# Performance work log

Hardware: AMD Instinct MI355X
Metric: run time of the kernel (lower is better)

Reference implementation:

```python
import jax, jax.numpy as jnp
import numpy as np

B, T, D, H = 1, 2049, 1024, 16
HD = D // H                      # head_dim = 64
MAX_SEQ = 1025
L = 2 * MAX_SEQ - 1              # = T (required by the module's relative shift)

def setup_inputs() -> dict:
    key = jax.random.key(0)
    ks = jax.random.split(key, 12)
    s = 0.02
    return {
        'q': jax.random.normal(ks[0], (B, T, D), dtype=jnp.float32),
        'k': jax.random.normal(ks[1], (B, T, D), dtype=jnp.float32),
        'v': jax.random.normal(ks[2], (B, T, D), dtype=jnp.float32),
        'mask': jnp.tril(jnp.ones((1, 1, T, T), dtype=jnp.int32)),  # causal
        'Wq_w': jax.random.normal(ks[3], (D, D), dtype=jnp.float32) * s,
        'Wq_b': jnp.zeros((D,), dtype=jnp.float32),
        'Wk_w': jax.random.normal(ks[4], (D, D), dtype=jnp.float32) * s,
        'Wk_b': jnp.zeros((D,), dtype=jnp.float32),
        'Wv_w': jax.random.normal(ks[5], (D, D), dtype=jnp.float32) * s,
        'Wv_b': jnp.zeros((D,), dtype=jnp.float32),
        'Er': jax.random.normal(ks[6], (L, HD), dtype=jnp.float32),
        'Wo_w': jax.random.normal(ks[7], (D, D), dtype=jnp.float32) * s,
        'Wo_b': jnp.zeros((D,), dtype=jnp.float32),
    }

def reference(q, k, v, mask, Wq_w, Wq_b, Wk_w, Wk_b, Wv_w, Wv_b, Er, Wo_w, Wo_b):
    b, t, d = q.shape
    def proj(x, w, bias):
        # nn.Linear: x @ W^T + b ; then (B,T,H,HD) -> (B,H,T,HD)
        return (x @ w.T + bias).reshape(b, t, H, HD).transpose(0, 2, 1, 3)
    qh = proj(q, Wq_w, Wq_b)
    kh = proj(k, Wk_w, Wk_b)
    vh = proj(v, Wv_w, Wv_b)
    scores = jnp.einsum('bhtd,bhsd->bhts', qh, kh)          # (B,H,T,T)
    QEr = jnp.einsum('bhtd,ld->bhtl', qh, Er)               # (B,H,T,L) with L == T
    # _relative_shift: pad a zero row on seq dim then drop first row ->
    # row i becomes QEr row i+1, last row zeros (faithful to torch code)
    rel = jnp.concatenate([QEr[:, :, 1:, :], jnp.zeros_like(QEr[:, :, :1, :])], axis=2)
    scores = scores + rel
    scores = jnp.where(mask[:, :, :t, :t] == 0, -jnp.inf, scores)
    attn = jax.nn.softmax(scores / (HD ** 0.5), axis=-1)
    ctx = jnp.einsum('bhts,bhsd->bthd', attn, vh).reshape(b, t, d)
    return ctx @ Wo_w.T + Wo_b
```

## Files before the change

kernel.cpp:

```cpp
#include <hip/hip_runtime.h>
#include <hip/hip_bf16.h>
#include <math.h>

constexpr int T_SEQ = 2049;
constexpr int D_MODEL = 1024;
constexpr int N_HEAD = 16;
constexpr int HEAD_DIM = 64;
constexpr int VT_STRIDE = 2112;
constexpr int T1_ROWS = 1152;

typedef __attribute__((ext_vector_type(8))) short short8;
typedef __attribute__((ext_vector_type(4))) short short4v;
typedef __attribute__((ext_vector_type(4))) float floatx4;

__device__ inline void load_lds16(const void* g, void* l) {
  __builtin_amdgcn_global_load_lds(
      (const __attribute__((address_space(1))) unsigned int*)g,
      (__attribute__((address_space(3))) unsigned int*)l, 16, 0, 0);
}

__device__ inline short8 cvt8_bf16(const float* p) {
  float4 a = *(const float4*)p, b = *(const float4*)(p + 4);
  __hip_bfloat16 t[8] = {__float2bfloat16(a.x), __float2bfloat16(a.y),
                         __float2bfloat16(a.z), __float2bfloat16(a.w),
                         __float2bfloat16(b.x), __float2bfloat16(b.y),
                         __float2bfloat16(b.z), __float2bfloat16(b.w)};
  return *(const short8*)t;
}

__device__ inline float bf2f(__hip_bfloat16 x) { return __bfloat162float(x); }

__global__ __launch_bounds__(256) void cast_all(
    const float* __restrict__ q, const float* __restrict__ k,
    const float* __restrict__ v, const float* __restrict__ wq,
    const float* __restrict__ wk, const float* __restrict__ wv,
    const float* __restrict__ wo, const float* __restrict__ er,
    __hip_bfloat16* __restrict__ qo, __hip_bfloat16* __restrict__ ko,
    __hip_bfloat16* __restrict__ vo, __hip_bfloat16* __restrict__ wqo,
    __hip_bfloat16* __restrict__ wko, __hip_bfloat16* __restrict__ wvo,
    __hip_bfloat16* __restrict__ woo, __hip_bfloat16* __restrict__ ero) {
  const int z = blockIdx.y;
  const float* in;
  __hip_bfloat16* out;
  int n;
  switch (z) {
    case 0: in = q; out = qo; n = T_SEQ * D_MODEL; break;
    case 1: in = k; out = ko; n = T_SEQ * D_MODEL; break;
    case 2: in = v; out = vo; n = T_SEQ * D_MODEL; break;
    case 3: in = wq; out = wqo; n = D_MODEL * D_MODEL; break;
    case 4: in = wk; out = wko; n = D_MODEL * D_MODEL; break;
    case 5: in = wv; out = wvo; n = D_MODEL * D_MODEL; break;
    case 6: in = wo; out = woo; n = D_MODEL * D_MODEL; break;
    default: in = er; out = ero; n = T_SEQ * HEAD_DIM; break;
  }
  const int i = (blockIdx.x * 256 + threadIdx.x) * 8;
  if (i + 8 > n) return;
  *(short8*)(out + i) = cvt8_bf16(in + i);
}

template <int BM, int BN, int OUTK>
__global__ __launch_bounds__(256) void mfma_gemm(
    const __hip_bfloat16* __restrict__ A0, const __hip_bfloat16* __restrict__ A1,
    const __hip_bfloat16* __restrict__ A2, const __hip_bfloat16* __restrict__ W0,
    const __hip_bfloat16* __restrict__ W1, const __hip_bfloat16* __restrict__ W2,
    const float* __restrict__ bias0, const float* __restrict__ bias1,
    const float* __restrict__ bias2, void* C0, void* C1, void* C2, int M) {
  constexpr int K = D_MODEL;
  constexpr int MT = BM / 32;
  constexpr int NT = BN / 32;
  __shared__ __align__(16) __hip_bfloat16 As[2][BM * 64];
  __shared__ __align__(16) __hip_bfloat16 Bs[2][BN * 64];

  const int z = blockIdx.z;
  const short* A = (const short*)(z == 0 ? A0 : z == 1 ? A1 : A2);
  const short* W = (const short*)(z == 0 ? W0 : z == 1 ? W1 : W2);
  const float* bias = z == 0 ? bias0 : z == 1 ? bias1 : bias2;
  void* C = z == 0 ? C0 : z == 1 ? C1 : C2;

  const int tid = threadIdx.x;
  const int wave = tid >> 6, lane = tid & 63;
  const int col = lane & 15, quad = lane >> 4;
  const int wm = wave >> 1, wn = wave & 1;
  const int m0 = blockIdx.y * BM, n0 = blockIdx.x * BN;

  const int srow = lane >> 3;
  const int sslot = lane & 7;
  const int sch = sslot ^ srow;

  floatx4 acc[MT][NT];
#pragma unroll
  for (int i = 0; i < MT; i++)
#pragma unroll
    for (int j = 0; j < NT; j++) acc[i][j] = (floatx4){0.f, 0.f, 0.f, 0.f};

#define GSTAGE(K0, BUF)                                                     \
  {                                                                         \
    _Pragma("unroll") for (int ii = 0; ii < BM / 32; ii++) {                \
      const int rb = (wave * (BM / 32) + ii) * 8;                           \
      const int am = min(m0 + rb + srow, M - 1);                            \
      load_lds16(A + (size_t)am * K + (K0) + sch * 8,                       \
                 (char*)&As[BUF][0] + rb * 128);                            \
    }                                                                       \
    _Pragma("unroll") for (int ii = 0; ii < BN / 32; ii++) {                \
      const int rb = (wave * (BN / 32) + ii) * 8;                           \
      const int bn = n0 + rb + srow;                                        \
      load_lds16(W + (size_t)bn * K + (K0) + sch * 8,                       \
                 (char*)&Bs[BUF][0] + rb * 128);                            \
    }                                                                       \
  }

  GSTAGE(0, 0)
  int buf = 0;

  for (int kb = 0; kb < K / 64; ++kb, buf ^= 1) {
    __syncthreads();
    if (kb + 1 < K / 64) GSTAGE((kb + 1) * 64, buf ^ 1)

    const __hip_bfloat16* as = &As[buf][0];
    const __hip_bfloat16* bs = &Bs[buf][0];
#pragma unroll
    for (int kk = 0; kk < 2; kk++) {
      short8 af[MT], bf[NT];
#pragma unroll
      for (int t = 0; t < MT; t++) {
        const int ra = wm * (BM / 2) + t * 16 + col;
        af[t] = *(const short8*)(as + ra * 64 + ((kk * 4 + quad) ^ (ra & 7)) * 8);
      }
#pragma unroll
      for (int t = 0; t < NT; t++) {
        const int rb = wn * (BN / 2) + t * 16 + col;
        bf[t] = *(const short8*)(bs + rb * 64 + ((kk * 4 + quad) ^ (rb & 7)) * 8);
      }
#pragma unroll
      for (int mt = 0; mt < MT; mt++)
#pragma unroll
        for (int nt = 0; nt < NT; nt++)
          acc[mt][nt] = __builtin_amdgcn_mfma_f32_16x16x32_bf16(af[mt], bf[nt],
                                                                acc[mt][nt], 0, 0, 0);
    }
  }

#pragma unroll
  for (int mt = 0; mt < MT; mt++) {
    const int mb = m0 + wm * (BM / 2) + mt * 16 + quad * 4;
#pragma unroll
    for (int nt = 0; nt < NT; nt++) {
      const int n = n0 + wn * (BN / 2) + nt * 16 + col;
      if (OUTK == 2 && z == 2) {
        __hip_bfloat16 pb[4];
#pragma unroll
        for (int r = 0; r < 4; r++)
          pb[r] = __float2bfloat16(acc[mt][nt][r] + bias[n]);
        __hip_bfloat16* vrow = (__hip_bfloat16*)C + (size_t)n * VT_STRIDE;
        if (mb + 4 <= M) {
          *(short4v*)(vrow + mb) = *(const short4v*)pb;
        } else {
#pragma unroll
          for (int r = 0; r < 4; r++)
            if (mb + r < M) vrow[mb + r] = pb[r];
        }
      } else {
#pragma unroll
        for (int r = 0; r < 4; r++) {
          const int m = mb + r;
          if (m >= M) continue;
          const float val = acc[mt][nt][r] + bias[n];
          if (OUTK == 0) {
            ((float*)C)[(size_t)m * D_MODEL + n] = val;
          } else {
            const int h = n >> 6, hd = n & 63;
            ((__hip_bfloat16*)C)[((size_t)h * T_SEQ + m) * HEAD_DIM + hd] =
                __float2bfloat16(val);
          }
        }
      }
    }
  }
}

__global__ __launch_bounds__(512, 4) void flash_attn(
    const __hip_bfloat16* __restrict__ qh, const __hip_bfloat16* __restrict__ kh,
    const __hip_bfloat16* __restrict__ er, const __hip_bfloat16* __restrict__ vt,
    __hip_bfloat16* __restrict__ ctx, __hip_bfloat16* __restrict__ O0,
    __hip_bfloat16* __restrict__ O1, float* __restrict__ l0g,
    float* __restrict__ l1g) {
  __shared__ __align__(16) __hip_bfloat16 Ks[2][64 * 128];
  __shared__ __align__(16) __hip_bfloat16 Vs[2][64 * 64];
  __shared__ __align__(16) __hip_bfloat16 Ps[8][1024];

  const int tid = threadIdx.x;
  const int h = blockIdx.y;
  const int b = blockIdx.x;

  const int qt = (b < 8) ? b : 8 + ((b - 8) >> 1);
  const int tq0 = qt * 128;
  const int jmax = min(tq0 + 127, T_SEQ - 1) >> 6;
  int j0, j1;
  bool alt;
  if (b < 8) {
    j0 = 0; j1 = jmax; alt = false;
  } else {
    const int mid = (jmax + 1) >> 1;
    alt = (b - 8) & 1;
    j0 = alt ? mid : 0;
    j1 = alt ? jmax : mid - 1;
  }

  const int wave = tid >> 6;
  const int lane = tid & 63;
  const int col = lane & 15;
  const int quad = lane >> 4;

  const short* qplane = (const short*)(qh + (size_t)h * T_SEQ * HEAD_DIM);
  const short* kplane = (const short*)(kh + (size_t)h * T_SEQ * HEAD_DIM);
  const short* eplane = (const short*)er;
  const short* vplane = (const short*)(vt + (size_t)h * HEAD_DIM * VT_STRIDE);

  const int t_abs = tq0 + wave * 16 + col;
  const int tload = min(t_abs, T_SEQ - 1);
  const bool hiz = (t_abs >= T_SEQ - 1);
  short8 aq[4];
#pragma unroll
  for (int kc = 0; kc < 4; kc++) {
    short8 v = *(const short8*)(qplane + (size_t)tload * 64 + kc * 32 + quad * 8);
    if (kc >= 2 && hiz) v = (short8){0, 0, 0, 0, 0, 0, 0, 0};
    aq[kc] = v;
  }

  floatx4 o[4];
  float l_lane = 0.f;
#pragma unroll
  for (int i = 0; i < 4; i++) o[i] = (floatx4){0.f, 0.f, 0.f, 0.f};

  const int tstrip = tq0 + wave * 16;
  __hip_bfloat16* psw = &Ps[wave][0];

#define STAGE_TILE(JJ, BUF)                                                        \
  {                                                                                \
    const int s0_ = (JJ) * 64;                                                     \
    _Pragma("unroll") for (int ii = 0; ii < 2; ii++) {                             \
      const int i_ = wave * 2 + ii;                                                \
      const int r_ = i_ * 4 + (lane >> 4);                                         \
      const int sl_ = lane & 15;                                                   \
      const int g_ = (sl_ & 8) | ((sl_ ^ (r_ & 7)) & 7);                           \
      const int s_ = min(s0_ + r_, T_SEQ - 1);                                     \
      const short* src_ = (g_ < 8) ? (kplane + (size_t)s_ * 64 + g_ * 8)           \
                                   : (eplane + (size_t)s_ * 64 + (g_ - 8) * 8);    \
      load_lds16(src_, (char*)&Ks[BUF][0] + i_ * 1024);                            \
    }                                                                              \
    {                                                                              \
      const int d_ = wave * 8 + (lane >> 3);                                       \
      const int sl_ = lane & 7;                                                    \
      const int g_ = sl_ ^ (d_ & 7);                                               \
      load_lds16(vplane + (size_t)d_ * VT_STRIDE + s0_ + g_ * 8,                   \
                 (char*)&Vs[BUF][0] + wave * 1024);                                \
    }                                                                              \
  }

  STAGE_TILE(j0, 0)
  int buf = 0;

  for (int j = j0; j <= j1; ++j, buf ^= 1) {
    __syncthreads();
    if (j < j1) STAGE_TILE(j + 1, buf ^ 1)

    const int s0 = j * 64;
    if (s0 > tstrip + 15) continue;

    const __hip_bfloat16* ks = &Ks[buf][0];
    const __hip_bfloat16* vs = &Vs[buf][0];

    floatx4 sacc[4];
#pragma unroll
    for (int st = 0; st < 4; st++) {
      floatx4 c = {0.f, 0.f, 0.f, 0.f};
      const int row = st * 16 + col;
#pragma unroll
      for (int kc = 0; kc < 4; kc++) {
        const int ch = kc * 4 + quad;
        const int slot = (ch & 8) | ((ch ^ (row & 7)) & 7);
        short8 ka = *(const short8*)(ks + row * 128 + slot * 8);
        c = __builtin_amdgcn_mfma_f32_16x16x32_bf16(ka, aq[kc], c, 0, 0, 0);
      }
      sacc[st] = c;
    }

    if (s0 + 63 > tstrip) {
#pragma unroll
      for (int st = 0; st < 4; st++) {
        const int sbase = s0 + st * 16 + quad * 4;
#pragma unroll
        for (int r = 0; r < 4; r++)
          if (sbase + r > t_abs) sacc[st][r] = -INFINITY;
      }
    }

    float rs = 0.f;
#pragma unroll
    for (int st = 0; st < 4; st++)
#pragma unroll
      for (int r = 0; r < 4; r++) {
        const float p = __expf(sacc[st][r] * 0.125f);
        sacc[st][r] = p;
        rs += p;
      }
    l_lane += rs;

#pragma unroll
    for (int st = 0; st < 4; st++) {
      __hip_bfloat16 pb[4];
#pragma unroll
      for (int r = 0; r < 4; r++) pb[r] = __float2bfloat16(sacc[st][r]);
      const int kcA = st >> 1;
      const int quadA = (st & 1) * 2 + (quad >> 1);
      const int off = ((kcA * 4 + quadA) * 16 + col) * 8 + (quad & 1) * 4;
      *(short4v*)(psw + off) = *(const short4v*)pb;
    }
    short8 pa[2];
#pragma unroll
    for (int kc = 0; kc < 2; kc++)
      pa[kc] = *(const short8*)(psw + ((kc * 4 + quad) * 16 + col) * 8);

#pragma unroll
    for (int nt = 0; nt < 4; nt++) {
      const int row = nt * 16 + col;
#pragma unroll
      for (int kc = 0; kc < 2; kc++) {
        const int slot = (kc * 4 + quad) ^ (row & 7);
        short8 vb = *(const short8*)(vs + row * 64 + slot * 8);
        o[nt] = __builtin_amdgcn_mfma_f32_16x16x32_bf16(pa[kc], vb, o[nt], 0, 0, 0);
      }
    }
  }

  l_lane += __shfl_xor(l_lane, 16, 64);
  l_lane += __shfl_xor(l_lane, 32, 64);

  if (b < 8) {
    const float linv = 1.0f / l_lane;
    float linv_r[4];
#pragma unroll
    for (int r = 0; r < 4; r++) linv_r[r] = __shfl(linv, quad * 4 + r, 64);
#pragma unroll
    for (int r = 0; r < 4; r++) {
      const int t = tstrip + quad * 4 + r;
#pragma unroll
      for (int nt = 0; nt < 4; nt++)
        ctx[(size_t)t * D_MODEL + h * 64 + nt * 16 + col] =
            __float2bfloat16(o[nt][r] * linv_r[r]);
    }
  } else {
    if (lane < 16) {
      const int t = tstrip + lane;
      if (t < T_SEQ) {
        if (!alt)
          l0g[h * T1_ROWS + (t - 1024)] = l_lane;
        else
          l1g[h * T1_ROWS + (t - 1024)] = l_lane;
      }
    }
#pragma unroll
    for (int r = 0; r < 4; r++) {
      const int t = tstrip + quad * 4 + r;
      if (t < T_SEQ) {
        __hip_bfloat16* dst = (!alt ? O0 : O1) + (size_t)(t - 1024) * D_MODEL;
#pragma unroll
        for (int nt = 0; nt < 4; nt++)
          dst[h * 64 + nt * 16 + col] = __float2bfloat16(o[nt][r]);
      }
    }
  }
}

__global__ __launch_bounds__(256) void finalize(
    const __hip_bfloat16* __restrict__ O0, const __hip_bfloat16* __restrict__ O1,
    const float* __restrict__ l0g, const float* __restrict__ l1g,
    __hip_bfloat16* __restrict__ ctx) {
  const int idx = blockIdx.x * 256 + threadIdx.x;
  const int tr = idx >> 7;
  const int t = 1024 + tr;
  if (t >= T_SEQ) return;
  const int ch = idx & 127;
  const int h = ch >> 3;

  const float l = l0g[h * T1_ROWS + tr] + l1g[h * T1_ROWS + tr];
  const __hip_bfloat16* a = O0 + (size_t)tr * D_MODEL + ch * 8;
  const __hip_bfloat16* bsrc = O1 + (size_t)tr * D_MODEL + ch * 8;
  const float inv = 1.0f / l;
  __hip_bfloat16 outv[8];
#pragma unroll
  for (int i = 0; i < 8; i++)
    outv[i] = __float2bfloat16((bf2f(a[i]) + bf2f(bsrc[i])) * inv);
  *(short8*)(ctx + (size_t)t * D_MODEL + ch * 8) = *(const short8*)outv;
}

extern "C" void kernel_launch(void* const* d_in, const int* in_sizes, int n_in,
                              void* d_out, int out_size, void* d_ws, size_t ws_size,
                              hipStream_t stream) {
  const float* q = (const float*)d_in[0];
  const float* k = (const float*)d_in[1];
  const float* v = (const float*)d_in[2];
  const float* Wq_w = (const float*)d_in[4];
  const float* Wq_b = (const float*)d_in[5];
  const float* Wk_w = (const float*)d_in[6];
  const float* Wk_b = (const float*)d_in[7];
  const float* Wv_w = (const float*)d_in[8];
  const float* Wv_b = (const float*)d_in[9];
  const float* Er = (const float*)d_in[10];
  const float* Wo_w = (const float*)d_in[11];
  const float* Wo_b = (const float*)d_in[12];
  float* out = (float*)d_out;

  char* p = (char*)d_ws;
  auto carve = [&](size_t bytes) {
    char* r = p;
    p += (bytes + 255) & ~(size_t)255;
    return r;
  };
  const size_t sz_plane = (size_t)T_SEQ * D_MODEL * 2;
  const size_t sz_w = (size_t)D_MODEL * D_MODEL * 2;
  __hip_bfloat16* qbf = (__hip_bfloat16*)carve(sz_plane);
  __hip_bfloat16* kbf = (__hip_bfloat16*)carve(sz_plane);
  __hip_bfloat16* vbf = (__hip_bfloat16*)carve(sz_plane);
  __hip_bfloat16* wqb = (__hip_bfloat16*)carve(sz_w);
  __hip_bfloat16* wkb = (__hip_bfloat16*)carve(sz_w);
  __hip_bfloat16* wvb = (__hip_bfloat16*)carve(sz_w);
  __hip_bfloat16* wob = (__hip_bfloat16*)carve(sz_w);
  __hip_bfloat16* qpr = (__hip_bfloat16*)carve(sz_plane);
  __hip_bfloat16* kpr = (__hip_bfloat16*)carve(sz_plane);
  __hip_bfloat16* vt =
      (__hip_bfloat16*)carve((size_t)N_HEAD * HEAD_DIM * VT_STRIDE * 2);
  __hip_bfloat16* er_bf = (__hip_bfloat16*)carve((size_t)T_SEQ * HEAD_DIM * 2);
  __hip_bfloat16* O0 = (__hip_bfloat16*)carve((size_t)T1_ROWS * D_MODEL * 2);
  __hip_bfloat16* O1 = (__hip_bfloat16*)carve((size_t)T1_ROWS * D_MODEL * 2);
  float* l0g = (float*)carve((size_t)N_HEAD * T1_ROWS * 4);
  float* l1g = (float*)carve((size_t)N_HEAD * T1_ROWS * 4);
  __hip_bfloat16* ctxb = (__hip_bfloat16*)carve(sz_plane);

  const dim3 blk(256);

  cast_all<<<dim3(1025, 8), blk, 0, stream>>>(q, k, v, Wq_w, Wk_w, Wv_w, Wo_w, Er,
                                              qbf, kbf, vbf, wqb, wkb, wvb, wob,
                                              er_bf);

  mfma_gemm<64, 128, 2><<<dim3(8, 33, 3), blk, 0, stream>>>(
      qbf, kbf, vbf, wqb, wkb, wvb, Wq_b, Wk_b, Wv_b, qpr, kpr, vt, T_SEQ);

  flash_attn<<<dim3(26, N_HEAD), dim3(512), 0, stream>>>(qpr, kpr, er_bf, vt, ctxb,
                                                         O0, O1, l0g, l1g);

  finalize<<<dim3((1025 * 128 + 255) / 256), blk, 0, stream>>>(O0, O1, l0g, l1g, ctxb);

  mfma_gemm<128, 64, 0><<<dim3(16, 17, 1), blk, 0, stream>>>(
      ctxb, ctxb, ctxb, wob, wob, wob, Wo_b, Wo_b, Wo_b, out, out, out, T_SEQ);
}
```

Measured before the change: 208.4 us.

## Fuse fp32-to-bf16 activation cast into QKV projection GEMM A-tile loads

The QKV projection GEMM now reads fp32 q/k/v directly, prefetches the next A tile into registers, converts to bf16 and writes to swizzled LDS, while weights still stream via global_load_lds. The separate cast pass over activations and its bf16 scratch planes are removed, and the weight cast kernel is shrunk accordingly. The QKV tile grows to 128x128, which halves block count and raises register pressure in exchange for more reuse. The output projection GEMM is simplified to a non-templated-output variant.

```diff
diff --git a/kernel.cpp b/kernel.cpp
--- a/kernel.cpp
+++ b/kernel.cpp
@@ -30,13 +30,10 @@
 
 __device__ inline float bf2f(__hip_bfloat16 x) { return __bfloat162float(x); }
 
-__global__ __launch_bounds__(256) void cast_all(
-    const float* __restrict__ q, const float* __restrict__ k,
-    const float* __restrict__ v, const float* __restrict__ wq,
-    const float* __restrict__ wk, const float* __restrict__ wv,
-    const float* __restrict__ wo, const float* __restrict__ er,
-    __hip_bfloat16* __restrict__ qo, __hip_bfloat16* __restrict__ ko,
-    __hip_bfloat16* __restrict__ vo, __hip_bfloat16* __restrict__ wqo,
+__global__ __launch_bounds__(256) void cast_w(
+    const float* __restrict__ wq, const float* __restrict__ wk,
+    const float* __restrict__ wv, const float* __restrict__ wo,
+    const float* __restrict__ er, __hip_bfloat16* __restrict__ wqo,
     __hip_bfloat16* __restrict__ wko, __hip_bfloat16* __restrict__ wvo,
     __hip_bfloat16* __restrict__ woo, __hip_bfloat16* __restrict__ ero) {
   const int z = blockIdx.y;
@@ -44,13 +41,10 @@
   __hip_bfloat16* out;
   int n;
   switch (z) {
-    case 0: in = q; out = qo; n = T_SEQ * D_MODEL; break;
-    case 1: in = k; out = ko; n = T_SEQ * D_MODEL; break;
-    case 2: in = v; out = vo; n = T_SEQ * D_MODEL; break;
-    case 3: in = wq; out = wqo; n = D_MODEL * D_MODEL; break;
-    case 4: in = wk; out = wko; n = D_MODEL * D_MODEL; break;
-    case 5: in = wv; out = wvo; n = D_MODEL * D_MODEL; break;
-    case 6: in = wo; out = woo; n = D_MODEL * D_MODEL; break;
+    case 0: in = wq; out = wqo; n = D_MODEL * D_MODEL; break;
+    case 1: in = wk; out = wko; n = D_MODEL * D_MODEL; break;
+    case 2: in = wv; out = wvo; n = D_MODEL * D_MODEL; break;
+    case 3: in = wo; out = woo; n = D_MODEL * D_MODEL; break;
     default: in = er; out = ero; n = T_SEQ * HEAD_DIM; break;
   }
   const int i = (blockIdx.x * 256 + threadIdx.x) * 8;
@@ -58,24 +52,142 @@
   *(short8*)(out + i) = cvt8_bf16(in + i);
 }
 
-template <int BM, int BN, int OUTK>
-__global__ __launch_bounds__(256) void mfma_gemm(
-    const __hip_bfloat16* __restrict__ A0, const __hip_bfloat16* __restrict__ A1,
-    const __hip_bfloat16* __restrict__ A2, const __hip_bfloat16* __restrict__ W0,
+__global__ __launch_bounds__(256) void qkv_gemm(
+    const float* __restrict__ A0, const float* __restrict__ A1,
+    const float* __restrict__ A2, const __hip_bfloat16* __restrict__ W0,
     const __hip_bfloat16* __restrict__ W1, const __hip_bfloat16* __restrict__ W2,
     const float* __restrict__ bias0, const float* __restrict__ bias1,
     const float* __restrict__ bias2, void* C0, void* C1, void* C2, int M) {
+  constexpr int K = D_MODEL;
+  __shared__ __align__(16) __hip_bfloat16 As[2][128 * 64];
+  __shared__ __align__(16) __hip_bfloat16 Bs[2][128 * 64];
+
+  const int z = blockIdx.z;
+  const float* A = z == 0 ? A0 : z == 1 ? A1 : A2;
+  const short* W = (const short*)(z == 0 ? W0 : z == 1 ? W1 : W2);
+  const float* bias = z == 0 ? bias0 : z == 1 ? bias1 : bias2;
+  void* C = z == 0 ? C0 : z == 1 ? C1 : C2;
+
+  const int tid = threadIdx.x;
+  const int wave = tid >> 6, lane = tid & 63;
+  const int col = lane & 15, quad = lane >> 4;
+  const int wm = wave >> 1, wn = wave & 1;
+  const int m0 = blockIdx.y * 128, n0 = blockIdx.x * 128;
+
+  const int srow = lane >> 3;
+  const int sslot = lane & 7;
+  const int sch = sslot ^ srow;
+
+  float Ra[4][8];
+
+#define ALOAD(K0)                                                        \
+  _Pragma("unroll") for (int ii = 0; ii < 4; ii++) {                     \
+    const int am = min(m0 + wave * 32 + ii * 8 + srow, M - 1);           \
+    const float* src_ = A + (size_t)am * K + (K0) + sch * 8;             \
+    *(float4*)&Ra[ii][0] = *(const float4*)src_;                         \
+    *(float4*)&Ra[ii][4] = *(const float4*)(src_ + 4);                   \
+  }
+
+#define AWRITE(BUF)                                                      \
+  _Pragma("unroll") for (int ii = 0; ii < 4; ii++) {                     \
+    const int r_ = wave * 32 + ii * 8 + srow;                            \
+    *(short8*)(&As[BUF][0] + r_ * 64 + sslot * 8) = cvt8_bf16(&Ra[ii][0]); \
+  }
+
+#define WSTAGE(K0, BUF)                                                  \
+  _Pragma("unroll") for (int ii = 0; ii < 4; ii++) {                     \
+    const int rb = (wave * 4 + ii) * 8;                                  \
+    const int bn = n0 + rb + srow;                                       \
+    load_lds16(W + (size_t)bn * K + (K0) + sch * 8,                      \
+               (char*)&Bs[BUF][0] + rb * 128);                           \
+  }
+
+  floatx4 acc[4][4];
+#pragma unroll
+  for (int i = 0; i < 4; i++)
+#pragma unroll
+    for (int j = 0; j < 4; j++) acc[i][j] = (floatx4){0.f, 0.f, 0.f, 0.f};
+
+  ALOAD(0)
+  AWRITE(0)
+  WSTAGE(0, 0)
+  ALOAD(64)
+
+  int buf = 0;
+  for (int kb = 0; kb < 16; ++kb, buf ^= 1) {
+    __syncthreads();
+    if (kb < 15) {
+      AWRITE(buf ^ 1)
+      WSTAGE((kb + 1) * 64, buf ^ 1)
+    }
+    if (kb < 14) ALOAD((kb + 2) * 64)
+
+    const __hip_bfloat16* as = &As[buf][0];
+    const __hip_bfloat16* bs = &Bs[buf][0];
+#pragma unroll
+    for (int kk = 0; kk < 2; kk++) {
+      short8 af[4], bf8[4];
+#pragma unroll
+      for (int t = 0; t < 4; t++) {
+        const int ra = wm * 64 + t * 16 + col;
+        af[t] = *(const short8*)(as + ra * 64 + ((kk * 4 + quad) ^ (ra & 7)) * 8);
+        const int rb = wn * 64 + t * 16 + col;
+        bf8[t] = *(const short8*)(bs + rb * 64 + ((kk * 4 + quad) ^ (rb & 7)) * 8);
+      }
+#pragma unroll
+      for (int mt = 0; mt < 4; mt++)
+#pragma unroll
+        for (int nt = 0; nt < 4; nt++)
+          acc[mt][nt] = __builtin_amdgcn_mfma_f32_16x16x32_bf16(af[mt], bf8[nt],
+                                                                acc[mt][nt], 0, 0, 0);
+    }
+  }
+
+#pragma unroll
+  for (int mt = 0; mt < 4; mt++) {
+    const int mb = m0 + wm * 64 + mt * 16 + quad * 4;
+#pragma unroll
+    for (int nt = 0; nt < 4; nt++) {
+      const int n = n0 + wn * 64 + nt * 16 + col;
+      if (z == 2) {
+        __hip_bfloat16 pb[4];
+#pragma unroll
+        for (int r = 0; r < 4; r++)
+          pb[r] = __float2bfloat16(acc[mt][nt][r] + bias[n]);
+        __hip_bfloat16* vrow = (__hip_bfloat16*)C + (size_t)n * VT_STRIDE;
+        if (mb + 4 <= M) {
+          *(short4v*)(vrow + mb) = *(const short4v*)pb;
+        } else {
+#pragma unroll
+          for (int r = 0; r < 4; r++)
+            if (mb + r < M) vrow[mb + r] = pb[r];
+        }
+      } else {
+        const int h = n >> 6, hd = n & 63;
+#pragma unroll
+        for (int r = 0; r < 4; r++) {
+          const int m = mb + r;
+          if (m >= M) continue;
+          ((__hip_bfloat16*)C)[((size_t)h * T_SEQ + m) * HEAD_DIM + hd] =
+              __float2bfloat16(acc[mt][nt][r] + bias[n]);
+        }
+      }
+    }
+  }
+}
+
+template <int BM, int BN>
+__global__ __launch_bounds__(256) void mfma_gemm(
+    const __hip_bfloat16* __restrict__ Ab, const __hip_bfloat16* __restrict__ Wb,
+    const float* __restrict__ bias, float* __restrict__ C, int M) {
   constexpr int K = D_MODEL;
   constexpr int MT = BM / 32;
   constexpr int NT = BN / 32;
   __shared__ __align__(16) __hip_bfloat16 As[2][BM * 64];
   __shared__ __align__(16) __hip_bfloat16 Bs[2][BN * 64];
 
-  const int z = blockIdx.z;
-  const short* A = (const short*)(z == 0 ? A0 : z == 1 ? A1 : A2);
-  const short* W = (const short*)(z == 0 ? W0 : z == 1 ? W1 : W2);
-  const float* bias = z == 0 ? bias0 : z == 1 ? bias1 : bias2;
-  void* C = z == 0 ? C0 : z == 1 ? C1 : C2;
+  const short* A = (const short*)Ab;
+  const short* W = (const short*)Wb;
 
   const int tid = threadIdx.x;
   const int wave = tid >> 6, lane = tid & 63;
@@ -120,7 +232,7 @@
     const __hip_bfloat16* bs = &Bs[buf][0];
 #pragma unroll
     for (int kk = 0; kk < 2; kk++) {
-      short8 af[MT], bf[NT];
+      short8 af[MT], bf8[NT];
 #pragma unroll
       for (int t = 0; t < MT; t++) {
         const int ra = wm * (BM / 2) + t * 16 + col;
@@ -129,13 +241,13 @@
 #pragma unroll
       for (int t = 0; t < NT; t++) {
         const int rb = wn * (BN / 2) + t * 16 + col;
-        bf[t] = *(const short8*)(bs + rb * 64 + ((kk * 4 + quad) ^ (rb & 7)) * 8);
+        bf8[t] = *(const short8*)(bs + rb * 64 + ((kk * 4 + quad) ^ (rb & 7)) * 8);
       }
 #pragma unroll
       for (int mt = 0; mt < MT; mt++)
 #pragma unroll
         for (int nt = 0; nt < NT; nt++)
-          acc[mt][nt] = __builtin_amdgcn_mfma_f32_16x16x32_bf16(af[mt], bf[nt],
+          acc[mt][nt] = __builtin_amdgcn_mfma_f32_16x16x32_bf16(af[mt], bf8[nt],
                                                                 acc[mt][nt], 0, 0, 0);
     }
   }
@@ -146,33 +258,11 @@
 #pragma unroll
     for (int nt = 0; nt < NT; nt++) {
       const int n = n0 + wn * (BN / 2) + nt * 16 + col;
-      if (OUTK == 2 && z == 2) {
-        __hip_bfloat16 pb[4];
-#pragma unroll
-        for (int r = 0; r < 4; r++)
-          pb[r] = __float2bfloat16(acc[mt][nt][r] + bias[n]);
-        __hip_bfloat16* vrow = (__hip_bfloat16*)C + (size_t)n * VT_STRIDE;
-        if (mb + 4 <= M) {
-          *(short4v*)(vrow + mb) = *(const short4v*)pb;
-        } else {
-#pragma unroll
-          for (int r = 0; r < 4; r++)
-            if (mb + r < M) vrow[mb + r] = pb[r];
-        }
-      } else {
-#pragma unroll
-        for (int r = 0; r < 4; r++) {
-          const int m = mb + r;
-          if (m >= M) continue;
-          const float val = acc[mt][nt][r] + bias[n];
-          if (OUTK == 0) {
-            ((float*)C)[(size_t)m * D_MODEL + n] = val;
-          } else {
-            const int h = n >> 6, hd = n & 63;
-            ((__hip_bfloat16*)C)[((size_t)h * T_SEQ + m) * HEAD_DIM + hd] =
-                __float2bfloat16(val);
-          }
-        }
+#pragma unroll
+      for (int r = 0; r < 4; r++) {
+        const int m = mb + r;
+        if (m >= M) continue;
+        C[(size_t)m * D_MODEL + n] = acc[mt][nt][r] + bias[n];
       }
     }
   }
@@ -419,9 +509,6 @@
   };
   const size_t sz_plane = (size_t)T_SEQ * D_MODEL * 2;
   const size_t sz_w = (size_t)D_MODEL * D_MODEL * 2;
-  __hip_bfloat16* qbf = (__hip_bfloat16*)carve(sz_plane);
-  __hip_bfloat16* kbf = (__hip_bfloat16*)carve(sz_plane);
-  __hip_bfloat16* vbf = (__hip_bfloat16*)carve(sz_plane);
   __hip_bfloat16* wqb = (__hip_bfloat16*)carve(sz_w);
   __hip_bfloat16* wkb = (__hip_bfloat16*)carve(sz_w);
   __hip_bfloat16* wvb = (__hip_bfloat16*)carve(sz_w);
@@ -439,18 +526,16 @@
 
   const dim3 blk(256);
 
-  cast_all<<<dim3(1025, 8), blk, 0, stream>>>(q, k, v, Wq_w, Wk_w, Wv_w, Wo_w, Er,
-                                              qbf, kbf, vbf, wqb, wkb, wvb, wob,
-                                              er_bf);
-
-  mfma_gemm<64, 128, 2><<<dim3(8, 33, 3), blk, 0, stream>>>(
-      qbf, kbf, vbf, wqb, wkb, wvb, Wq_b, Wk_b, Wv_b, qpr, kpr, vt, T_SEQ);
+  cast_w<<<dim3(512, 5), blk, 0, stream>>>(Wq_w, Wk_w, Wv_w, Wo_w, Er, wqb, wkb,
+                                           wvb, wob, er_bf);
+
+  qkv_gemm<<<dim3(8, 17, 3), blk, 0, stream>>>(q, k, v, wqb, wkb, wvb, Wq_b, Wk_b,
+                                               Wv_b, qpr, kpr, vt, T_SEQ);
 
   flash_attn<<<dim3(26, N_HEAD), dim3(512), 0, stream>>>(qpr, kpr, er_bf, vt, ctxb,
                                                          O0, O1, l0g, l1g);
 
   finalize<<<dim3((1025 * 128 + 255) / 256), blk, 0, stream>>>(O0, O1, l0g, l1g, ctxb);
 
-  mfma_gemm<128, 64, 0><<<dim3(16, 17, 1), blk, 0, stream>>>(
-      ctxb, ctxb, ctxb, wob, wob, wob, Wo_b, Wo_b, Wo_b, out, out, out, T_SEQ);
-}
+  mfma_gemm<128, 64><<<dim3(16, 17), blk, 0, stream>>>(ctxb, wob, Wo_b, out, T_SEQ);
+}
```

New measurement: 209.9 us. No clear change (+0.7%).
